# Kernel tuning notes

Hardware: AMD Instinct MI355X
Metric: run time of the kernel (lower is better)

The kernel has to match this reference:

```python
import jax, jax.numpy as jnp
import numpy as np

SQUARE_SIZE = 32
BATCH, CH, H, W = 256, 3, 224, 224


def setup_inputs() -> dict:
    key = jax.random.key(0)
    k1, k2, k3 = jax.random.split(key, 3)
    img = jax.random.normal(k1, (BATCH, CH, H, W), dtype=jnp.float32)
    hi = H - SQUARE_SIZE + 1  # 193
    y_idx = jax.random.randint(k2, (BATCH,), 0, hi, dtype=jnp.int32)
    x_idx = jax.random.randint(k3, (BATCH,), 0, hi, dtype=jnp.int32)
    return {"img": img, "y_idx": y_idx, "x_idx": x_idx}


def reference(img, y_idx, x_idx):
    # img: [B, C, H, W]; y_idx/x_idx: [B] top-left corners of zeroed square.
    B, C, H, W = img.shape
    rows = jnp.arange(H, dtype=jnp.int32)  # [H]
    cols = jnp.arange(W, dtype=jnp.int32)  # [W]
    # in_y: [B, H], in_x: [B, W]
    in_y = (rows[None, :] >= y_idx[:, None]) & (rows[None, :] < y_idx[:, None] + SQUARE_SIZE)
    in_x = (cols[None, :] >= x_idx[:, None]) & (cols[None, :] < x_idx[:, None] + SQUARE_SIZE)
    # square region -> mask 0, else 1; broadcast over channels
    in_square = in_y[:, None, :, None] & in_x[:, None, None, :]  # [B, 1, H, W]
    mask = jnp.where(in_square, jnp.float32(0.0), jnp.float32(1.0))
    return img * mask
```

## Files before the change

kernel.cpp:

```cpp
#include <hip/hip_runtime.h>


#define SQ 32
#define B_ 256
#define C_ 3
#define H_ 224
#define W_ 224

__global__ __launch_bounds__(256) void rsd_kernel(const float4* __restrict__ img,
                                                  const int* __restrict__ y_idx,
                                                  const int* __restrict__ x_idx,
                                                  float4* __restrict__ out,
                                                  int total4) {
    int i4 = blockIdx.x * 256 + threadIdx.x;
    if (i4 >= total4) return;

    float4 v = img[i4];

    int i = i4 << 2;
    int w = i % W_;
    int t = i / W_;
    int h = t % H_;
    int b = t / (C_ * H_);

    int y0 = y_idx[b];
    int x0 = x_idx[b];

    bool row_in = (h >= y0) & (h < y0 + SQ);
    if (row_in) {
        if ((w + 0) >= x0 && (w + 0) < x0 + SQ) v.x = 0.0f;
        if ((w + 1) >= x0 && (w + 1) < x0 + SQ) v.y = 0.0f;
        if ((w + 2) >= x0 && (w + 2) < x0 + SQ) v.z = 0.0f;
        if ((w + 3) >= x0 && (w + 3) < x0 + SQ) v.w = 0.0f;
    }

    out[i4] = v;
}

extern "C" void kernel_launch(void* const* d_in, const int* in_sizes, int n_in,
                              void* d_out, int out_size, void* d_ws, size_t ws_size,
                              hipStream_t stream) {
    const float4* img  = (const float4*)d_in[0];
    const int*    yidx = (const int*)d_in[1];
    const int*    xidx = (const int*)d_in[2];
    float4*       out  = (float4*)d_out;

    int total4 = out_size / 4;
    int blocks = (total4 + 255) / 256;
    rsd_kernel<<<blocks, 256, 0, stream>>>(img, yidx, xidx, out, total4);
}
```

Before: 254.6 us.

## Split into a plain copy kernel plus a per-image square-zeroing kernel

Replaces the fused masked copy with two launches: a pure float4 copy with four elements per thread, and a second kernel with one block per image that writes zeros over the 3x32x32 square. This drops the per-element div/mod index math and the per-sample index loads from the bandwidth-bound copy. It adds a second launch and a serialized dependency, plus scattered scalar writes that rewrite data the copy just stored.

Result: slower. 268.7 us (+5.6%).

```diff
diff --git a/kernel.cpp b/kernel.cpp
--- a/kernel.cpp
+++ b/kernel.cpp
@@ -6,35 +6,34 @@
 #define C_ 3
 #define H_ 224
 #define W_ 224
+#define IMG_ELEMS (C_ * H_ * W_)
 
-__global__ __launch_bounds__(256) void rsd_kernel(const float4* __restrict__ img,
-                                                  const int* __restrict__ y_idx,
-                                                  const int* __restrict__ x_idx,
-                                                  float4* __restrict__ out,
-                                                  int total4) {
-    int i4 = blockIdx.x * 256 + threadIdx.x;
-    if (i4 >= total4) return;
+__global__ __launch_bounds__(256) void copy_kernel(const float4* __restrict__ src,
+                                                   float4* __restrict__ dst,
+                                                   int total4) {
+    int base = blockIdx.x * (256 * 4) + threadIdx.x;
+#pragma unroll
+    for (int k = 0; k < 4; ++k) {
+        int i = base + k * 256;
+        if (i < total4) dst[i] = src[i];
+    }
+}
 
-    float4 v = img[i4];
-
-    int i = i4 << 2;
-    int w = i % W_;
-    int t = i / W_;
-    int h = t % H_;
-    int b = t / (C_ * H_);
-
+__global__ __launch_bounds__(256) void zero_kernel(const int* __restrict__ y_idx,
+                                                   const int* __restrict__ x_idx,
+                                                   float* __restrict__ out) {
+    int b  = blockIdx.x;
     int y0 = y_idx[b];
     int x0 = x_idx[b];
-
-    bool row_in = (h >= y0) & (h < y0 + SQ);
-    if (row_in) {
-        if ((w + 0) >= x0 && (w + 0) < x0 + SQ) v.x = 0.0f;
-        if ((w + 1) >= x0 && (w + 1) < x0 + SQ) v.y = 0.0f;
-        if ((w + 2) >= x0 && (w + 2) < x0 + SQ) v.z = 0.0f;
-        if ((w + 3) >= x0 && (w + 3) < x0 + SQ) v.w = 0.0f;
+    float* img = out + (size_t)b * IMG_ELEMS;
+#pragma unroll
+    for (int t = 0; t < 12; ++t) {
+        int idx = t * 256 + threadIdx.x;
+        int c   = idx >> 10;
+        int dy  = (idx >> 5) & 31;
+        int dx  = idx & 31;
+        img[(c * H_ + y0 + dy) * W_ + x0 + dx] = 0.0f;
     }
-
-    out[i4] = v;
 }
 
 extern "C" void kernel_launch(void* const* d_in, const int* in_sizes, int n_in,
@@ -43,9 +42,9 @@
     const float4* img  = (const float4*)d_in[0];
     const int*    yidx = (const int*)d_in[1];
     const int*    xidx = (const int*)d_in[2];
-    float4*       out  = (float4*)d_out;
 
     int total4 = out_size / 4;
-    int blocks = (total4 + 255) / 256;
-    rsd_kernel<<<blocks, 256, 0, stream>>>(img, yidx, xidx, out, total4);
+    int blocks = (total4 + (256 * 4) - 1) / (256 * 4);
+    copy_kernel<<<blocks, 256, 0, stream>>>(img, (float4*)d_out, total4);
+    zero_kernel<<<B_, 256, 0, stream>>>(yidx, xidx, (float*)d_out);
 }
```
